# Kernel tuning notes

Hardware: AMD Instinct MI355X
Metric: run time of the kernel (lower is better)

## Reference

```python
import jax, jax.numpy as jnp
import numpy as np
from jax import lax

B, CI, CO, H, W = 8, 64, 64, 256, 256
M1 = M2 = 16
RANK, NEXP, SCALING = 4, 15, 0.1
G = 4  # expert_region_size = sqrt(num_experts + 1)
WF = W // 2 + 1

# expert i occupies grid cell (row, col) = ((i+1)//G, (i+1)%G); cell (0,0) is the base weights1 corner
_IDX = np.arange(1, NEXP + 1)
RR = jnp.asarray(_IDX // G)
CC = jnp.asarray(_IDX % G)


def setup_inputs() -> dict:
    key = jax.random.key(0)
    ks = jax.random.split(key, 20)
    rn = lambda k, shape, s: jax.random.normal(k, shape, jnp.float32) * s
    scale = 1.0 / (CI * CO)
    return {
        "x": rn(ks[0], (B, CI, H, W), 1.0),
        "w1_re": jax.random.uniform(ks[1], (CI, CO, M1, M2), jnp.float32) * scale,
        "w1_im": jax.random.uniform(ks[2], (CI, CO, M1, M2), jnp.float32) * scale,
        "w2_re": jax.random.uniform(ks[3], (CI, CO, M1, M2), jnp.float32) * scale,
        "w2_im": jax.random.uniform(ks[4], (CI, CO, M1, M2), jnp.float32) * scale,
        "la1_re": rn(ks[5], (NEXP, RANK, CI), 0.02),
        "la1_im": rn(ks[6], (NEXP, RANK, CI), 0.02),
        "lb1_re": rn(ks[7], (NEXP, CO, RANK, M1, M2), 0.02),
        "lb1_im": rn(ks[8], (NEXP, CO, RANK, M1, M2), 0.02),
        "la2_re": rn(ks[9], (NEXP, RANK, CI), 0.02),
        "la2_im": rn(ks[10], (NEXP, RANK, CI), 0.02),
        "lb2_re": rn(ks[11], (NEXP, CO, RANK, M1, M2), 0.02),
        "lb2_im": rn(ks[12], (NEXP, CO, RANK, M1, M2), 0.02),
        "gate1": rn(ks[13], (NEXP,), 0.1),
        "gate2": rn(ks[14], (NEXP,), 0.1),
    }


def reference(x, w1_re, w1_im, w2_re, w2_im,
              la1_re, la1_im, lb1_re, lb1_im,
              la2_re, la2_im, lb2_re, lb2_im,
              gate1, gate2):
    x_ft = jnp.fft.rfft2(x)  # [B, CI, H, WF] complex64

    # scalar gates (gate_on_data=False): sigmoid(gate / temperature), temperature=1
    g1 = jax.nn.sigmoid(gate1)  # [E]
    g2 = jax.nn.sigmoid(gate2)
    sploss = jnp.mean(g1) + jnp.mean(g2)

    w1 = lax.complex(w1_re, w1_im)
    w2 = lax.complex(w2_re, w2_im)
    la1 = lax.complex(la1_re, la1_im)
    lb1 = lax.complex(lb1_re, lb1_im)
    la2 = lax.complex(la2_re, la2_im)
    lb2 = lax.complex(lb2_re, lb2_im)

    # per-expert LoRA weights: sum_r lora_b[o,r,x,y] * lora_a[r,i] -> [E, I, O, M1, M2]
    lw1 = jnp.einsum("eri,eorxy->eioxy", la1, lb1) * SCALING
    lw2 = jnp.einsum("eri,eorxy->eioxy", la2, lb2) * SCALING

    # base corner products
    top_base = jnp.einsum("bixy,ioxy->boxy", x_ft[:, :, :M1, :M2], w1)
    bot_base = jnp.einsum("bixy,ioxy->boxy", x_ft[:, :, H - M1:, :M2], w2)

    # gather all expert input tiles at once via a GxG grid view of the low-freq corners
    top = x_ft[:, :, :G * M1, :G * M2].reshape(B, CI, G, M1, G, M2)
    topt = jnp.transpose(top, (2, 4, 0, 1, 3, 5))        # [G, G, B, CI, M1, M2]
    xe1 = topt[RR, CC]                                    # [E, B, CI, M1, M2]
    bot = x_ft[:, :, H - G * M1:, :G * M2].reshape(B, CI, G, M1, G, M2)
    bott = jnp.transpose(bot, (2, 4, 0, 1, 3, 5))
    xe2 = bott[G - 1 - RR, CC]  # rows H-row_end:H-row_start == bottom-grid block 3-row_idx

    oe1 = jnp.einsum("ebixy,eioxy->eboxy", xe1, lw1) * g1[:, None, None, None, None]
    oe2 = jnp.einsum("ebixy,eioxy->eboxy", xe2, lw2) * g2[:, None, None, None, None]

    # scatter all disjoint tiles back into out_ft
    out_top = jnp.zeros((G, G, B, CO, M1, M2), jnp.complex64)
    out_top = out_top.at[0, 0].set(top_base).at[RR, CC].set(oe1)
    out_bot = jnp.zeros((G, G, B, CO, M1, M2), jnp.complex64)
    out_bot = out_bot.at[G - 1, 0].set(bot_base).at[G - 1 - RR, CC].set(oe2)

    out_ft = jnp.zeros((B, CO, H, WF), jnp.complex64)
    top_full = jnp.transpose(out_top, (2, 3, 0, 4, 1, 5)).reshape(B, CO, G * M1, G * M2)
    bot_full = jnp.transpose(out_bot, (2, 3, 0, 4, 1, 5)).reshape(B, CO, G * M1, G * M2)
    out_ft = out_ft.at[:, :, :G * M1, :G * M2].set(top_full)
    out_ft = out_ft.at[:, :, H - G * M1:, :G * M2].set(bot_full)

    y = jnp.fft.irfft2(out_ft, s=(H, W))
    return (y, sploss)
```

## Files before the change

kernel.cpp:

```cpp
#include <hip/hip_runtime.h>
#include <math.h>

#define B_   8
#define CI_  64
#define CO_  64
#define H_   256
#define W_   256
#define NE_  15
#define RK_  4

typedef __attribute__((ext_vector_type(8))) short short8;
typedef __attribute__((ext_vector_type(4))) float f32x4;

__device__ __forceinline__ unsigned bf16u(float f) {
  return (__float_as_uint(f) + 0x8000u) >> 16;
}
__device__ __forceinline__ unsigned pk2(float lo, float hi) {
  return ((__float_as_uint(lo) + 0x8000u) >> 16) |
         ((__float_as_uint(hi) + 0x8000u) & 0xFFFF0000u);
}
__device__ __forceinline__ float ubf(unsigned short u) {
  return __uint_as_float(((unsigned)u) << 16);
}

__global__ __launch_bounds__(256) void kTab(unsigned short* __restrict__ TAt,
                                            unsigned short* __restrict__ TB,
                                            unsigned short* __restrict__ TD,
                                            unsigned short* __restrict__ TEt) {
  int idx = blockIdx.x * 256 + threadIdx.x;
  const float C = 6.28318530717958647692f / 256.f;
  if (idx < 32768) {
    int n = idx >> 8, q = idx & 255;
    int w = n >> 1, pl = n & 1;
    int mm = (q * w) & 255;
    float s, c; sincosf(C * (float)mm, &s, &c);
    TAt[idx] = (unsigned short)bf16u(pl ? -s : c);
    return;
  }
  idx -= 32768;
  if (idx < 131072) {
    int mrow = idx >> 9, k = idx & 511;
    int p = k >> 1, tt = k & 1;
    int hr = mrow & 127, imr = mrow >> 7;
    int h = (hr < 64) ? hr : hr + 128;
    int mm = (p * h) & 255;
    float s, c; sincosf(C * (float)mm, &s, &c);
    float v = (imr == 0) ? (tt == 0 ? c : s) : (tt == 0 ? -s : c);
    TB[idx] = (unsigned short)bf16u(v);
    return;
  }
  idx -= 131072;
  if (idx < 131072) {
    int mrow = idx >> 8, k = idx & 255;
    int hr = k >> 1, tt = k & 1;
    int p = mrow & 255, imr = mrow >> 8;
    int h = (hr < 64) ? hr : hr + 128;
    int mm = (p * h) & 255;
    float s, c; sincosf(C * (float)mm, &s, &c);
    float v = (imr == 0) ? (tt == 0 ? c : -s) : (tt == 0 ? s : c);
    TD[idx] = (unsigned short)bf16u(v);
    return;
  }
  idx -= 131072;
  if (idx < 32768) {
    int q = idx >> 7, k = idx & 127;
    int w = k >> 1, pl = k & 1;
    int mm = (q * w) & 255;
    float s, c; sincosf(C * (float)mm, &s, &c);
    float v = (pl == 0) ? ((w == 0 ? 1.f : 2.f * c) / 65536.f)
                        : ((w == 0 ? 0.f : -2.f * s) / 65536.f);
    TEt[idx] = (unsigned short)bf16u(v);
  }
}

__global__ __launch_bounds__(512, 4) void kAB(const float* __restrict__ x,
                                              const unsigned short* __restrict__ TAt,
                                              const unsigned short* __restrict__ TB,
                                              unsigned short* __restrict__ Xf) {
  __shared__ unsigned short As[256 * 32];
  __shared__ unsigned short Bs1[128 * 32];
  __shared__ unsigned short XcL[64 * 264];
  int t = threadIdx.x, lane = t & 63, wid = t >> 6;
  int bi = blockIdx.x;
  const float* xb = x + (size_t)bi * 65536;
  int lrow = lane & 15, lk = (lane >> 4) * 8;
  f32x4 acc2[2][4];
#pragma unroll
  for (int a = 0; a < 2; ++a)
#pragma unroll
    for (int b = 0; b < 4; ++b) acc2[a][b] = (f32x4){0.f, 0.f, 0.f, 0.f};

  for (int half = 0; half < 2; ++half) {
    f32x4 acc1[2][4];
#pragma unroll
    for (int a = 0; a < 2; ++a)
#pragma unroll
      for (int b = 0; b < 4; ++b) acc1[a][b] = (f32x4){0.f, 0.f, 0.f, 0.f};
    int mb1 = (wid >> 1) * 32, nb1 = (wid & 1) * 64;
    for (int kk = 0; kk < 8; ++kk) {
      int k0 = kk * 32;
      __syncthreads();
      {
        int r = t >> 2, hf = t & 3;
        const float* xp = xb + (size_t)(half * 128 + r) * 256 + k0 + hf * 8;
        float4 v0 = *(const float4*)(xp);
        float4 v1 = *(const float4*)(xp + 4);
        uint4 o;
        o.x = pk2(v0.x, v0.y); o.y = pk2(v0.z, v0.w);
        o.z = pk2(v1.x, v1.y); o.w = pk2(v1.z, v1.w);
        *(uint4*)&As[r * 32 + hf * 8] = o;
      }
      {
        int n = t >> 2, seg = t & 3;
        *(uint4*)&Bs1[n * 32 + seg * 8] = *(const uint4*)&TAt[n * 256 + k0 + seg * 8];
      }
      __syncthreads();
      short8 af[2], bf[4];
#pragma unroll
      for (int a = 0; a < 2; ++a)
        af[a] = *(const short8*)&As[(mb1 + a * 16 + lrow) * 32 + lk];
#pragma unroll
      for (int b = 0; b < 4; ++b)
        bf[b] = *(const short8*)&Bs1[(nb1 + b * 16 + lrow) * 32 + lk];
#pragma unroll
      for (int a = 0; a < 2; ++a)
#pragma unroll
        for (int b = 0; b < 4; ++b)
          acc1[a][b] = __builtin_amdgcn_mfma_f32_16x16x32_bf16(af[a], bf[b], acc1[a][b], 0, 0, 0);
    }
    __syncthreads();
#pragma unroll
    for (int a = 0; a < 2; ++a)
#pragma unroll
      for (int b = 0; b < 4; ++b)
#pragma unroll
        for (int r = 0; r < 4; ++r) {
          int m = mb1 + a * 16 + (lane >> 4) * 4 + r;
          int n = nb1 + b * 16 + lrow;
          XcL[(n >> 1) * 264 + 2 * m + (n & 1)] = (unsigned short)bf16u(acc1[a][b][r]);
        }
    __syncthreads();
    int mb2 = wid * 32;
    for (int kk = 0; kk < 8; ++kk) {
      int k0 = kk * 32;
      __syncthreads();
#pragma unroll
      for (int j = 0; j < 2; ++j) {
        int c = j * 512 + t;
        int m = c >> 2, seg = c & 3;
        *(uint4*)&As[m * 32 + seg * 8] =
            *(const uint4*)&TB[m * 512 + half * 256 + k0 + seg * 8];
      }
      __syncthreads();
      short8 af2[2], bf2[4];
#pragma unroll
      for (int a = 0; a < 2; ++a)
        af2[a] = *(const short8*)&As[(mb2 + a * 16 + lrow) * 32 + lk];
#pragma unroll
      for (int b = 0; b < 4; ++b)
        bf2[b] = *(const short8*)&XcL[(b * 16 + lrow) * 264 + k0 + lk];
#pragma unroll
      for (int a = 0; a < 2; ++a)
#pragma unroll
        for (int b = 0; b < 4; ++b)
          acc2[a][b] = __builtin_amdgcn_mfma_f32_16x16x32_bf16(af2[a], bf2[b], acc2[a][b], 0, 0, 0);
    }
  }
  unsigned short* dst = Xf + (size_t)bi * 16384;
#pragma unroll
  for (int a = 0; a < 2; ++a)
#pragma unroll
    for (int b = 0; b < 4; ++b)
#pragma unroll
      for (int r = 0; r < 4; ++r) {
        int m = wid * 32 + a * 16 + (lane >> 4) * 4 + r;
        int n = b * 16 + lrow;
        dst[m * 64 + n] = (unsigned short)bf16u(acc2[a][b][r]);
      }
}

__global__ __launch_bounds__(256) void kT(const unsigned short* __restrict__ Xf,
                                          float2* __restrict__ T,
                                          const float* __restrict__ la1re,
                                          const float* __restrict__ la1im,
                                          const float* __restrict__ la2re,
                                          const float* __restrict__ la2im) {
  int bid = blockIdx.x;
  int b = bid & 7;
  int e = (bid >> 3) % 15;
  int reg = bid / 120;
  int ep1 = e + 1;
  int grr = (reg == 0) ? (ep1 >> 2) : (3 - (ep1 >> 2));
  int gc = ep1 & 3;
  int hr0 = reg * 64 + grr * 16;
  int w0 = gc * 16;
  int t = threadIdx.x;
  int xx = t >> 4, yy = t & 15;
  const unsigned short* xp =
      Xf + (size_t)b * 64 * 16384 + (hr0 + xx) * 64 + (w0 + yy);
  const float* lare = (reg == 0) ? la1re : la2re;
  const float* laim = (reg == 0) ? la1im : la2im;
  float ar0 = 0.f, ai0 = 0.f, ar1 = 0.f, ai1 = 0.f;
  float ar2 = 0.f, ai2 = 0.f, ar3 = 0.f, ai3 = 0.f;
  for (int i = 0; i < 64; ++i) {
    float xr = ubf(xp[(size_t)i * 16384]);
    float xi = ubf(xp[(size_t)i * 16384 + 8192]);
    float l0r = lare[(e * 4 + 0) * 64 + i], l0i = laim[(e * 4 + 0) * 64 + i];
    float l1r = lare[(e * 4 + 1) * 64 + i], l1i = laim[(e * 4 + 1) * 64 + i];
    float l2r = lare[(e * 4 + 2) * 64 + i], l2i = laim[(e * 4 + 2) * 64 + i];
    float l3r = lare[(e * 4 + 3) * 64 + i], l3i = laim[(e * 4 + 3) * 64 + i];
    ar0 += l0r * xr - l0i * xi; ai0 += l0r * xi + l0i * xr;
    ar1 += l1r * xr - l1i * xi; ai1 += l1r * xi + l1i * xr;
    ar2 += l2r * xr - l2i * xi; ai2 += l2r * xi + l2i * xr;
    ar3 += l3r * xr - l3i * xi; ai3 += l3r * xi + l3i * xr;
  }
  float2* dst = T + ((((size_t)reg * 15 + e) * 8 + b) * 256 + t) * 4;
  dst[0] = make_float2(ar0, ai0);
  dst[1] = make_float2(ar1, ai1);
  dst[2] = make_float2(ar2, ai2);
  dst[3] = make_float2(ar3, ai3);
}

__global__ __launch_bounds__(256) void kDM(const unsigned short* __restrict__ Xf,
                                           const float2* __restrict__ T,
                                           unsigned short* __restrict__ Gt,
                                           const float* __restrict__ w1re,
                                           const float* __restrict__ w1im,
                                           const float* __restrict__ w2re,
                                           const float* __restrict__ w2im,
                                           const float* __restrict__ lb1re,
                                           const float* __restrict__ lb1im,
                                           const float* __restrict__ lb2re,
                                           const float* __restrict__ lb2im,
                                           const float* __restrict__ gate1,
                                           const float* __restrict__ gate2) {
  __shared__ unsigned Xs[32 * 4 * 8 * 8];
  if (blockIdx.x < 256) {
    int bid = blockIdx.x;
    int yc = bid & 1, xc = (bid >> 1) & 3, oc = (bid >> 3) & 15, reg = bid >> 7;
    int hrb = (reg == 0) ? xc * 4 : 112 + xc * 4;
    const float* Wre = (reg == 0) ? w1re : w2re;
    const float* Wim = (reg == 0) ? w1im : w2im;
    int t = threadIdx.x;
    int b = t >> 5, o = (t >> 3) & 3, yy = t & 7;
    int og = oc * 4 + o, yyg = yc * 8 + yy;
    float ar[4] = {0.f, 0.f, 0.f, 0.f}, ai[4] = {0.f, 0.f, 0.f, 0.f};
    for (int ch = 0; ch < 2; ++ch) {
      __syncthreads();
#pragma unroll
      for (int j = 0; j < 4; ++j) {
        int seg = t + j * 256;
        int sb = seg >> 7, sx = (seg >> 5) & 3, si = seg & 31;
        int i = ch * 32 + si;
        const unsigned short* p =
            Xf + (size_t)(sb * 64 + i) * 16384 + (hrb + sx) * 64 + yc * 8;
        uint4 re = *(const uint4*)p;
        uint4 im = *(const uint4*)(p + 8192);
        uint4 o0, o1;
        o0.x = (re.x & 0xFFFFu) | (im.x << 16);
        o0.y = (re.x >> 16) | (im.x & 0xFFFF0000u);
        o0.z = (re.y & 0xFFFFu) | (im.y << 16);
        o0.w = (re.y >> 16) | (im.y & 0xFFFF0000u);
        o1.x = (re.z & 0xFFFFu) | (im.z << 16);
        o1.y = (re.z >> 16) | (im.z & 0xFFFF0000u);
        o1.z = (re.w & 0xFFFFu) | (im.w << 16);
        o1.w = (re.w >> 16) | (im.w & 0xFFFF0000u);
        uint4* d = (uint4*)&Xs[((si * 4 + sx) * 8 + sb) * 8];
        d[0] = o0; d[1] = o1;
      }
      __syncthreads();
      for (int ic = 0; ic < 32; ++ic) {
        int i = ch * 32 + ic;
#pragma unroll
        for (int xs = 0; xs < 4; ++xs) {
          unsigned pk = Xs[((ic * 4 + xs) * 8 + b) * 8 + yy];
          float xr = ubf((unsigned short)(pk & 0xFFFFu));
          float xi = ubf((unsigned short)(pk >> 16));
          int widx = ((i * 64 + og) * 16 + xc * 4 + xs) * 16 + yyg;
          float wr = Wre[widx], wi = Wim[widx];
          ar[xs] += xr * wr - xi * wi;
          ai[xs] += xr * wi + xi * wr;
        }
      }
    }
    uint4 ov;
    ov.x = pk2(ar[0], ai[0]);
    ov.y = pk2(ar[1], ai[1]);
    ov.z = pk2(ar[2], ai[2]);
    ov.w = pk2(ar[3], ai[3]);
    *(uint4*)(Gt + ((size_t)(b * 64 + og) * 64 + yyg) * 256 + 2 * hrb) = ov;
  } else {
    int bid = blockIdx.x - 256;
    int xc = bid & 3, hrc = (bid >> 2) & 7, oc = bid >> 5;
    int t = threadIdx.x;
    int w = t & 63, og = t >> 6;
    int o = oc * 4 + og;
    int reg = hrc >> 2;
    int grr = hrc & 3;
    int gc = w >> 4, yy = w & 15;
    int e = (reg == 0) ? (4 * grr + gc - 1) : (4 * (3 - grr) + gc - 1);
    if (e < 0) return;
    float gate = (reg == 0) ? gate1[e] : gate2[e];
    float g = 0.1f / (1.f + __expf(-gate));
    const float* lbre = (reg == 0) ? lb1re : lb2re;
    const float* lbim = (reg == 0) ? lb1im : lb2im;
    size_t lbb = ((size_t)(e * 64 + o) * 4) * 256 + yy;
    float blr[4][4], bli[4][4];
#pragma unroll
    for (int x2 = 0; x2 < 4; ++x2) {
      int xx = xc * 4 + x2;
      const float* pr = lbre + lbb + xx * 16;
      const float* pi = lbim + lbb + xx * 16;
#pragma unroll
      for (int r = 0; r < 4; ++r) {
        blr[x2][r] = pr[r * 256];
        bli[x2][r] = pi[r * 256];
      }
    }
    const size_t tbase = (((size_t)reg * 15 + e) * 8) * 256 + yy;
    for (int b = 0; b < 8; ++b) {
      const float4* tp = (const float4*)(T + (tbase + (size_t)b * 256) * 4);
      unsigned out4[4];
#pragma unroll
      for (int x2 = 0; x2 < 4; ++x2) {
        int xx = xc * 4 + x2;
        float4 t01 = tp[xx * 32];
        float4 t23 = tp[xx * 32 + 1];
        float ar = 0.f, aim = 0.f;
        ar += t01.x * blr[x2][0] - t01.y * bli[x2][0];
        aim += t01.x * bli[x2][0] + t01.y * blr[x2][0];
        ar += t01.z * blr[x2][1] - t01.w * bli[x2][1];
        aim += t01.z * bli[x2][1] + t01.w * blr[x2][1];
        ar += t23.x * blr[x2][2] - t23.y * bli[x2][2];
        aim += t23.x * bli[x2][2] + t23.y * blr[x2][2];
        ar += t23.z * blr[x2][3] - t23.w * bli[x2][3];
        aim += t23.z * bli[x2][3] + t23.w * blr[x2][3];
        out4[x2] = pk2(g * ar, g * aim);
      }
      *(uint4*)(Gt + ((size_t)(b * 64 + o) * 64 + w) * 256 + hrc * 32 + xc * 8) =
          make_uint4(out4[0], out4[1], out4[2], out4[3]);
    }
  }
}

__global__ __launch_bounds__(512, 4) void kDE(const unsigned short* __restrict__ Gt,
                                              const unsigned short* __restrict__ TD,
                                              const unsigned short* __restrict__ TEt,
                                              float* __restrict__ y) {
  __shared__ __align__(16) char smem[77824];
  unsigned short* As  = (unsigned short*)smem;
  unsigned short* Bs  = (unsigned short*)(smem + 32768);
  unsigned short* ZL  = (unsigned short*)smem;
  unsigned short* Bs2 = (unsigned short*)(smem + 69632);
  int t = threadIdx.x, lane = t & 63, wid = t >> 6;
  int bo = blockIdx.x;
  const unsigned short* Grow = Gt + (size_t)bo * 16384;
  int lrow = lane & 15, lk = (lane >> 4) * 8;

  {
    int mb = wid * 64;
    f32x4 acc[4][4];
#pragma unroll
    for (int a = 0; a < 4; ++a)
#pragma unroll
      for (int b = 0; b < 4; ++b) acc[a][b] = (f32x4){0.f, 0.f, 0.f, 0.f};
    for (int kk = 0; kk < 8; ++kk) {
      int k0 = kk * 32;
      __syncthreads();
#pragma unroll
      for (int j = 0; j < 4; ++j) {
        int c = j * 512 + t;
        int m = c >> 2, seg = c & 3;
        *(uint4*)&As[m * 32 + seg * 8] = *(const uint4*)&TD[m * 256 + k0 + seg * 8];
      }
      if (t < 256) {
        int n = t >> 2, seg = t & 3;
        *(uint4*)&Bs[n * 32 + seg * 8] = *(const uint4*)&Grow[n * 256 + k0 + seg * 8];
      }
      __syncthreads();
      short8 af[4], bf[4];
#pragma unroll
      for (int a = 0; a < 4; ++a)
        af[a] = *(const short8*)&As[(mb + a * 16 + lrow) * 32 + lk];
#pragma unroll
      for (int b = 0; b < 4; ++b)
        bf[b] = *(const short8*)&Bs[(b * 16 + lrow) * 32 + lk];
#pragma unroll
      for (int a = 0; a < 4; ++a)
#pragma unroll
        for (int b = 0; b < 4; ++b)
          acc[a][b] = __builtin_amdgcn_mfma_f32_16x16x32_bf16(af[a], bf[b], acc[a][b], 0, 0, 0);
    }
    __syncthreads();
#pragma unroll
    for (int a = 0; a < 4; ++a)
#pragma unroll
      for (int b = 0; b < 4; ++b)
#pragma unroll
        for (int r = 0; r < 4; ++r) {
          int m = mb + a * 16 + (lane >> 4) * 4 + r;
          int p = m & 255, pl = m >> 8;
          int n = b * 16 + lrow;
          ZL[p * 136 + 2 * n + pl] = (unsigned short)bf16u(acc[a][b][r]);
        }
    __syncthreads();
  }

  int mb2 = (wid >> 1) * 64, nb2 = (wid & 1) * 64;
  for (int qh = 0; qh < 2; ++qh) {
    f32x4 acc[4][4];
#pragma unroll
    for (int a = 0; a < 4; ++a)
#pragma unroll
      for (int b = 0; b < 4; ++b) acc[a][b] = (f32x4){0.f, 0.f, 0.f, 0.f};
    for (int kk = 0; kk < 4; ++kk) {
      int k0 = kk * 32;
      __syncthreads();
      {
        int n = t >> 2, seg = t & 3;
        *(uint4*)&Bs2[n * 32 + seg * 8] =
            *(const uint4*)&TEt[(qh * 128 + n) * 128 + k0 + seg * 8];
      }
      __syncthreads();
      short8 af[4], bf[4];
#pragma unroll
      for (int a = 0; a < 4; ++a)
        af[a] = *(const short8*)&ZL[(mb2 + a * 16 + lrow) * 136 + k0 + lk];
#pragma unroll
      for (int b = 0; b < 4; ++b)
        bf[b] = *(const short8*)&Bs2[(nb2 + b * 16 + lrow) * 32 + lk];
#pragma unroll
      for (int a = 0; a < 4; ++a)
#pragma unroll
        for (int b = 0; b < 4; ++b)
          acc[a][b] = __builtin_amdgcn_mfma_f32_16x16x32_bf16(af[a], bf[b], acc[a][b], 0, 0, 0);
    }
    float* dst = y + (size_t)bo * 65536 + qh * 128;
#pragma unroll
    for (int a = 0; a < 4; ++a)
#pragma unroll
      for (int b = 0; b < 4; ++b)
#pragma unroll
        for (int r = 0; r < 4; ++r) {
          int p = mb2 + a * 16 + (lane >> 4) * 4 + r;
          int q = nb2 + b * 16 + lrow;
          dst[(size_t)p * 256 + q] = acc[a][b][r];
        }
  }
}

__global__ void kS2(const float* __restrict__ gate1, const float* __restrict__ gate2,
                    float* __restrict__ out) {
  if (threadIdx.x == 0) {
    float s = 0.f;
    for (int e = 0; e < NE_; ++e)
      s += 1.f / (1.f + expf(-gate1[e])) + 1.f / (1.f + expf(-gate2[e]));
    out[0] = s / (float)NE_;
  }
}

extern "C" void kernel_launch(void* const* d_in, const int* in_sizes, int n_in,
                              void* d_out, int out_size, void* d_ws, size_t ws_size,
                              hipStream_t stream) {
  const float* x     = (const float*)d_in[0];
  const float* w1re  = (const float*)d_in[1];
  const float* w1im  = (const float*)d_in[2];
  const float* w2re  = (const float*)d_in[3];
  const float* w2im  = (const float*)d_in[4];
  const float* la1re = (const float*)d_in[5];
  const float* la1im = (const float*)d_in[6];
  const float* lb1re = (const float*)d_in[7];
  const float* lb1im = (const float*)d_in[8];
  const float* la2re = (const float*)d_in[9];
  const float* la2im = (const float*)d_in[10];
  const float* lb2re = (const float*)d_in[11];
  const float* lb2im = (const float*)d_in[12];
  const float* gate1 = (const float*)d_in[13];
  const float* gate2 = (const float*)d_in[14];

  char* ws = (char*)d_ws;
  unsigned short* Xf  = (unsigned short*)(ws + ((size_t)32 << 20));
  unsigned short* Gt  = (unsigned short*)(ws + ((size_t)48 << 20));
  unsigned short* TAt = (unsigned short*)(ws + ((size_t)96 << 20));
  unsigned short* TB  = TAt + 32768;
  unsigned short* TD  = TB + 131072;
  unsigned short* TEt = TD + 131072;
  float2* Tw = (float2*)(ws + ((size_t)97 << 20));
  float* y = (float*)d_out;

  kTab<<<1280, 256, 0, stream>>>(TAt, TB, TD, TEt);
  kAB<<<512, 512, 0, stream>>>(x, TAt, TB, Xf);
  kT<<<240, 256, 0, stream>>>(Xf, Tw, la1re, la1im, la2re, la2im);
  kDM<<<768, 256, 0, stream>>>(Xf, Tw, Gt, w1re, w1im, w2re, w2im,
                               lb1re, lb1im, lb2re, lb2im, gate1, gate2);
  kDE<<<512, 512, 0, stream>>>(Gt, TD, TEt, y);
  kS2<<<1, 64, 0, stream>>>(gate1, gate2, y + (size_t)B_ * CO_ * H_ * W_);
}
```

Measured before the change: 395.9 us.

## Load MFMA operands directly from global memory, dropping LDS staging and barriers

In kAB and kDE the MFMA fragments are now read straight from global memory (twiddle tables, input x, Gt) rather than staged through shared-memory tiles guarded by __syncthreads in every k-step. kAB's first GEMM is regridded so each wave owns 16 rows across all 128 columns, converting x to bf16 in registers. The change removes LDS round trips and barriers but leans on L1/L2 caching for operand reuse across waves, with less coalesced 16-byte loads. It also drops the min-blocks launch bound and unrolls kC's reduction loop by 8.

New measurement: 471.9 us. +19.2%, slower.

```diff
diff --git a/kernel.cpp b/kernel.cpp
--- a/kernel.cpp
+++ b/kernel.cpp
@@ -73,12 +73,10 @@
   }
 }
 
-__global__ __launch_bounds__(512, 4) void kAB(const float* __restrict__ x,
-                                              const unsigned short* __restrict__ TAt,
-                                              const unsigned short* __restrict__ TB,
-                                              unsigned short* __restrict__ Xf) {
-  __shared__ unsigned short As[256 * 32];
-  __shared__ unsigned short Bs1[128 * 32];
+__global__ __launch_bounds__(512) void kAB(const float* __restrict__ x,
+                                           const unsigned short* __restrict__ TAt,
+                                           const unsigned short* __restrict__ TB,
+                                           unsigned short* __restrict__ Xf) {
   __shared__ unsigned short XcL[64 * 264];
   int t = threadIdx.x, lane = t & 63, wid = t >> 6;
   int bi = blockIdx.x;
@@ -91,71 +89,41 @@
     for (int b = 0; b < 4; ++b) acc2[a][b] = (f32x4){0.f, 0.f, 0.f, 0.f};
 
   for (int half = 0; half < 2; ++half) {
-    f32x4 acc1[2][4];
-#pragma unroll
-    for (int a = 0; a < 2; ++a)
-#pragma unroll
-      for (int b = 0; b < 4; ++b) acc1[a][b] = (f32x4){0.f, 0.f, 0.f, 0.f};
-    int mb1 = (wid >> 1) * 32, nb1 = (wid & 1) * 64;
+    f32x4 acc1[8];
+#pragma unroll
+    for (int b = 0; b < 8; ++b) acc1[b] = (f32x4){0.f, 0.f, 0.f, 0.f};
+    const float* xrow = xb + (size_t)(half * 128 + wid * 16 + lrow) * 256 + lk;
     for (int kk = 0; kk < 8; ++kk) {
       int k0 = kk * 32;
-      __syncthreads();
-      {
-        int r = t >> 2, hf = t & 3;
-        const float* xp = xb + (size_t)(half * 128 + r) * 256 + k0 + hf * 8;
-        float4 v0 = *(const float4*)(xp);
-        float4 v1 = *(const float4*)(xp + 4);
-        uint4 o;
-        o.x = pk2(v0.x, v0.y); o.y = pk2(v0.z, v0.w);
-        o.z = pk2(v1.x, v1.y); o.w = pk2(v1.z, v1.w);
-        *(uint4*)&As[r * 32 + hf * 8] = o;
-      }
-      {
-        int n = t >> 2, seg = t & 3;
-        *(uint4*)&Bs1[n * 32 + seg * 8] = *(const uint4*)&TAt[n * 256 + k0 + seg * 8];
-      }
-      __syncthreads();
-      short8 af[2], bf[4];
-#pragma unroll
-      for (int a = 0; a < 2; ++a)
-        af[a] = *(const short8*)&As[(mb1 + a * 16 + lrow) * 32 + lk];
-#pragma unroll
-      for (int b = 0; b < 4; ++b)
-        bf[b] = *(const short8*)&Bs1[(nb1 + b * 16 + lrow) * 32 + lk];
-#pragma unroll
-      for (int a = 0; a < 2; ++a)
-#pragma unroll
-        for (int b = 0; b < 4; ++b)
-          acc1[a][b] = __builtin_amdgcn_mfma_f32_16x16x32_bf16(af[a], bf[b], acc1[a][b], 0, 0, 0);
+      float4 v0 = *(const float4*)(xrow + k0);
+      float4 v1 = *(const float4*)(xrow + k0 + 4);
+      union { short8 s; unsigned u[4]; } afu;
+      afu.u[0] = pk2(v0.x, v0.y); afu.u[1] = pk2(v0.z, v0.w);
+      afu.u[2] = pk2(v1.x, v1.y); afu.u[3] = pk2(v1.z, v1.w);
+      short8 af = afu.s;
+#pragma unroll
+      for (int b = 0; b < 8; ++b) {
+        short8 bf = *(const short8*)&TAt[(b * 16 + lrow) * 256 + k0 + lk];
+        acc1[b] = __builtin_amdgcn_mfma_f32_16x16x32_bf16(af, bf, acc1[b], 0, 0, 0);
+      }
     }
     __syncthreads();
 #pragma unroll
-    for (int a = 0; a < 2; ++a)
-#pragma unroll
-      for (int b = 0; b < 4; ++b)
-#pragma unroll
-        for (int r = 0; r < 4; ++r) {
-          int m = mb1 + a * 16 + (lane >> 4) * 4 + r;
-          int n = nb1 + b * 16 + lrow;
-          XcL[(n >> 1) * 264 + 2 * m + (n & 1)] = (unsigned short)bf16u(acc1[a][b][r]);
-        }
+    for (int b = 0; b < 8; ++b)
+#pragma unroll
+      for (int r = 0; r < 4; ++r) {
+        int m = wid * 16 + (lane >> 4) * 4 + r;
+        int n = b * 16 + lrow;
+        XcL[(n >> 1) * 264 + 2 * m + (n & 1)] = (unsigned short)bf16u(acc1[b][r]);
+      }
     __syncthreads();
     int mb2 = wid * 32;
     for (int kk = 0; kk < 8; ++kk) {
       int k0 = kk * 32;
-      __syncthreads();
-#pragma unroll
-      for (int j = 0; j < 2; ++j) {
-        int c = j * 512 + t;
-        int m = c >> 2, seg = c & 3;
-        *(uint4*)&As[m * 32 + seg * 8] =
-            *(const uint4*)&TB[m * 512 + half * 256 + k0 + seg * 8];
-      }
-      __syncthreads();
       short8 af2[2], bf2[4];
 #pragma unroll
       for (int a = 0; a < 2; ++a)
-        af2[a] = *(const short8*)&As[(mb2 + a * 16 + lrow) * 32 + lk];
+        af2[a] = *(const short8*)&TB[(mb2 + a * 16 + lrow) * 512 + half * 256 + k0 + lk];
 #pragma unroll
       for (int b = 0; b < 4; ++b)
         bf2[b] = *(const short8*)&XcL[(b * 16 + lrow) * 264 + k0 + lk];
@@ -202,6 +170,7 @@
   const float* laim = (reg == 0) ? la1im : la2im;
   float ar0 = 0.f, ai0 = 0.f, ar1 = 0.f, ai1 = 0.f;
   float ar2 = 0.f, ai2 = 0.f, ar3 = 0.f, ai3 = 0.f;
+#pragma unroll 8
   for (int i = 0; i < 64; ++i) {
     float xr = ubf(xp[(size_t)i * 16384]);
     float xi = ubf(xp[(size_t)i * 16384 + 8192]);
@@ -343,15 +312,11 @@
   }
 }
 
-__global__ __launch_bounds__(512, 4) void kDE(const unsigned short* __restrict__ Gt,
-                                              const unsigned short* __restrict__ TD,
-                                              const unsigned short* __restrict__ TEt,
-                                              float* __restrict__ y) {
-  __shared__ __align__(16) char smem[77824];
-  unsigned short* As  = (unsigned short*)smem;
-  unsigned short* Bs  = (unsigned short*)(smem + 32768);
-  unsigned short* ZL  = (unsigned short*)smem;
-  unsigned short* Bs2 = (unsigned short*)(smem + 69632);
+__global__ __launch_bounds__(512) void kDE(const unsigned short* __restrict__ Gt,
+                                           const unsigned short* __restrict__ TD,
+                                           const unsigned short* __restrict__ TEt,
+                                           float* __restrict__ y) {
+  __shared__ unsigned short ZL[256 * 136];
   int t = threadIdx.x, lane = t & 63, wid = t >> 6;
   int bo = blockIdx.x;
   const unsigned short* Grow = Gt + (size_t)bo * 16384;
@@ -366,32 +331,19 @@
       for (int b = 0; b < 4; ++b) acc[a][b] = (f32x4){0.f, 0.f, 0.f, 0.f};
     for (int kk = 0; kk < 8; ++kk) {
       int k0 = kk * 32;
-      __syncthreads();
-#pragma unroll
-      for (int j = 0; j < 4; ++j) {
-        int c = j * 512 + t;
-        int m = c >> 2, seg = c & 3;
-        *(uint4*)&As[m * 32 + seg * 8] = *(const uint4*)&TD[m * 256 + k0 + seg * 8];
-      }
-      if (t < 256) {
-        int n = t >> 2, seg = t & 3;
-        *(uint4*)&Bs[n * 32 + seg * 8] = *(const uint4*)&Grow[n * 256 + k0 + seg * 8];
-      }
-      __syncthreads();
       short8 af[4], bf[4];
 #pragma unroll
       for (int a = 0; a < 4; ++a)
-        af[a] = *(const short8*)&As[(mb + a * 16 + lrow) * 32 + lk];
+        af[a] = *(const short8*)&TD[(mb + a * 16 + lrow) * 256 + k0 + lk];
 #pragma unroll
       for (int b = 0; b < 4; ++b)
-        bf[b] = *(const short8*)&Bs[(b * 16 + lrow) * 32 + lk];
+        bf[b] = *(const short8*)&Grow[(b * 16 + lrow) * 256 + k0 + lk];
 #pragma unroll
       for (int a = 0; a < 4; ++a)
 #pragma unroll
         for (int b = 0; b < 4; ++b)
           acc[a][b] = __builtin_amdgcn_mfma_f32_16x16x32_bf16(af[a], bf[b], acc[a][b], 0, 0, 0);
     }
-    __syncthreads();
 #pragma unroll
     for (int a = 0; a < 4; ++a)
 #pragma unroll
@@ -415,20 +367,13 @@
       for (int b = 0; b < 4; ++b) acc[a][b] = (f32x4){0.f, 0.f, 0.f, 0.f};
     for (int kk = 0; kk < 4; ++kk) {
       int k0 = kk * 32;
-      __syncthreads();
-      {
-        int n = t >> 2, seg = t & 3;
-        *(uint4*)&Bs2[n * 32 + seg * 8] =
-            *(const uint4*)&TEt[(qh * 128 + n) * 128 + k0 + seg * 8];
-      }
-      __syncthreads();
       short8 af[4], bf[4];
 #pragma unroll
       for (int a = 0; a < 4; ++a)
         af[a] = *(const short8*)&ZL[(mb2 + a * 16 + lrow) * 136 + k0 + lk];
 #pragma unroll
       for (int b = 0; b < 4; ++b)
-        bf[b] = *(const short8*)&Bs2[(nb2 + b * 16 + lrow) * 32 + lk];
+        bf[b] = *(const short8*)&TEt[(qh * 128 + nb2 + b * 16 + lrow) * 128 + k0 + lk];
 #pragma unroll
       for (int a = 0; a < 4; ++a)
 #pragma unroll
```

## Use direct global-to-LDS loads with XOR-swizzled tiles and K=64 steps in DFT GEMMs

Applied to the files above, without the earlier changes.

Table and spectrum tiles in kAB and kDE are now loaded with the global_load_lds builtin, so they go straight to shared memory instead of through registers. Tiles are stored with an XOR swizzle to avoid LDS bank conflicts. kAB now takes K in steps of 64, which halves the number of barrier pairs, and the minimum-occupancy launch bound is dropped. Together these aim to cut LDS conflicts, VGPR staging and synchronisation overhead, at the cost of more complex addressing and possibly lower occupancy.

After: 387.2 us. -2.2%, faster.

```diff
diff --git a/kernel.cpp b/kernel.cpp
--- a/kernel.cpp
+++ b/kernel.cpp
@@ -21,6 +21,11 @@
 }
 __device__ __forceinline__ float ubf(unsigned short u) {
   return __uint_as_float(((unsigned)u) << 16);
+}
+__device__ __forceinline__ void gload16(const void* g, void* l) {
+  __builtin_amdgcn_global_load_lds(
+      (const __attribute__((address_space(1))) unsigned int*)g,
+      (__attribute__((address_space(3))) unsigned int*)l, 16, 0, 0);
 }
 
 __global__ __launch_bounds__(256) void kTab(unsigned short* __restrict__ TAt,
@@ -73,17 +78,16 @@
   }
 }
 
-__global__ __launch_bounds__(512, 4) void kAB(const float* __restrict__ x,
-                                              const unsigned short* __restrict__ TAt,
-                                              const unsigned short* __restrict__ TB,
-                                              unsigned short* __restrict__ Xf) {
-  __shared__ unsigned short As[256 * 32];
-  __shared__ unsigned short Bs1[128 * 32];
+__global__ __launch_bounds__(512) void kAB(const float* __restrict__ x,
+                                           const unsigned short* __restrict__ TAt,
+                                           const unsigned short* __restrict__ TB,
+                                           unsigned short* __restrict__ Xf) {
+  __shared__ unsigned short As[16384];
   __shared__ unsigned short XcL[64 * 264];
   int t = threadIdx.x, lane = t & 63, wid = t >> 6;
   int bi = blockIdx.x;
   const float* xb = x + (size_t)bi * 65536;
-  int lrow = lane & 15, lk = (lane >> 4) * 8;
+  int lrow = lane & 15, lk = (lane >> 4) * 8, jhi = lane >> 4;
   f32x4 acc2[2][4];
 #pragma unroll
   for (int a = 0; a < 2; ++a)
@@ -97,36 +101,46 @@
 #pragma unroll
       for (int b = 0; b < 4; ++b) acc1[a][b] = (f32x4){0.f, 0.f, 0.f, 0.f};
     int mb1 = (wid >> 1) * 32, nb1 = (wid & 1) * 64;
-    for (int kk = 0; kk < 8; ++kk) {
-      int k0 = kk * 32;
-      __syncthreads();
-      {
-        int r = t >> 2, hf = t & 3;
-        const float* xp = xb + (size_t)(half * 128 + r) * 256 + k0 + hf * 8;
-        float4 v0 = *(const float4*)(xp);
-        float4 v1 = *(const float4*)(xp + 4);
-        uint4 o;
-        o.x = pk2(v0.x, v0.y); o.y = pk2(v0.z, v0.w);
-        o.z = pk2(v1.x, v1.y); o.w = pk2(v1.z, v1.w);
-        *(uint4*)&As[r * 32 + hf * 8] = o;
-      }
-      {
-        int n = t >> 2, seg = t & 3;
-        *(uint4*)&Bs1[n * 32 + seg * 8] = *(const uint4*)&TAt[n * 256 + k0 + seg * 8];
-      }
-      __syncthreads();
-      short8 af[2], bf[4];
-#pragma unroll
-      for (int a = 0; a < 2; ++a)
-        af[a] = *(const short8*)&As[(mb1 + a * 16 + lrow) * 32 + lk];
-#pragma unroll
-      for (int b = 0; b < 4; ++b)
-        bf[b] = *(const short8*)&Bs1[(nb1 + b * 16 + lrow) * 32 + lk];
-#pragma unroll
-      for (int a = 0; a < 2; ++a)
-#pragma unroll
-        for (int b = 0; b < 4; ++b)
-          acc1[a][b] = __builtin_amdgcn_mfma_f32_16x16x32_bf16(af[a], bf[b], acc1[a][b], 0, 0, 0);
+    for (int kk = 0; kk < 4; ++kk) {
+      int k0 = kk * 64;
+      __syncthreads();
+#pragma unroll
+      for (int j = 0; j < 2; ++j) {
+        int c = j * 512 + t;
+        int r = c >> 3, seg = c & 7;
+        int ssw = (seg ^ (r & 7)) * 8;
+        {
+          const float* xp = xb + (size_t)(half * 128 + r) * 256 + k0 + ssw;
+          float4 v0 = *(const float4*)(xp);
+          float4 v1 = *(const float4*)(xp + 4);
+          uint4 o;
+          o.x = pk2(v0.x, v0.y); o.y = pk2(v0.z, v0.w);
+          o.z = pk2(v1.x, v1.y); o.w = pk2(v1.z, v1.w);
+          *(uint4*)&As[r * 64 + seg * 8] = o;
+        }
+        gload16(&TAt[r * 256 + k0 + ssw], &As[8192 + c * 8]);
+      }
+      __syncthreads();
+#pragma unroll
+      for (int k2 = 0; k2 < 64; k2 += 32) {
+        int jb = (k2 >> 3) + jhi;
+        short8 af[2], bf[4];
+#pragma unroll
+        for (int a = 0; a < 2; ++a) {
+          int row = mb1 + a * 16 + lrow;
+          af[a] = *(const short8*)&As[row * 64 + ((jb ^ (row & 7))) * 8];
+        }
+#pragma unroll
+        for (int b = 0; b < 4; ++b) {
+          int row = nb1 + b * 16 + lrow;
+          bf[b] = *(const short8*)&As[8192 + row * 64 + ((jb ^ (row & 7))) * 8];
+        }
+#pragma unroll
+        for (int a = 0; a < 2; ++a)
+#pragma unroll
+          for (int b = 0; b < 4; ++b)
+            acc1[a][b] = __builtin_amdgcn_mfma_f32_16x16x32_bf16(af[a], bf[b], acc1[a][b], 0, 0, 0);
+      }
     }
     __syncthreads();
 #pragma unroll
@@ -141,29 +155,35 @@
         }
     __syncthreads();
     int mb2 = wid * 32;
-    for (int kk = 0; kk < 8; ++kk) {
-      int k0 = kk * 32;
-      __syncthreads();
-#pragma unroll
-      for (int j = 0; j < 2; ++j) {
+    for (int kk = 0; kk < 4; ++kk) {
+      int k0 = kk * 64;
+      __syncthreads();
+#pragma unroll
+      for (int j = 0; j < 4; ++j) {
         int c = j * 512 + t;
-        int m = c >> 2, seg = c & 3;
-        *(uint4*)&As[m * 32 + seg * 8] =
-            *(const uint4*)&TB[m * 512 + half * 256 + k0 + seg * 8];
-      }
-      __syncthreads();
-      short8 af2[2], bf2[4];
-#pragma unroll
-      for (int a = 0; a < 2; ++a)
-        af2[a] = *(const short8*)&As[(mb2 + a * 16 + lrow) * 32 + lk];
-#pragma unroll
-      for (int b = 0; b < 4; ++b)
-        bf2[b] = *(const short8*)&XcL[(b * 16 + lrow) * 264 + k0 + lk];
-#pragma unroll
-      for (int a = 0; a < 2; ++a)
+        int m = c >> 3, seg = c & 7;
+        int ssw = (seg ^ (m & 7)) * 8;
+        gload16(&TB[m * 512 + half * 256 + k0 + ssw], &As[c * 8]);
+      }
+      __syncthreads();
+#pragma unroll
+      for (int k2 = 0; k2 < 64; k2 += 32) {
+        int jb = (k2 >> 3) + jhi;
+        short8 af2[2], bf2[4];
+#pragma unroll
+        for (int a = 0; a < 2; ++a) {
+          int row = mb2 + a * 16 + lrow;
+          af2[a] = *(const short8*)&As[row * 64 + ((jb ^ (row & 7))) * 8];
+        }
 #pragma unroll
         for (int b = 0; b < 4; ++b)
-          acc2[a][b] = __builtin_amdgcn_mfma_f32_16x16x32_bf16(af2[a], bf2[b], acc2[a][b], 0, 0, 0);
+          bf2[b] = *(const short8*)&XcL[(b * 16 + lrow) * 264 + k0 + k2 + lk];
+#pragma unroll
+        for (int a = 0; a < 2; ++a)
+#pragma unroll
+          for (int b = 0; b < 4; ++b)
+            acc2[a][b] = __builtin_amdgcn_mfma_f32_16x16x32_bf16(af2[a], bf2[b], acc2[a][b], 0, 0, 0);
+      }
     }
   }
   unsigned short* dst = Xf + (size_t)bi * 16384;
@@ -202,6 +222,7 @@
   const float* laim = (reg == 0) ? la1im : la2im;
   float ar0 = 0.f, ai0 = 0.f, ar1 = 0.f, ai1 = 0.f;
   float ar2 = 0.f, ai2 = 0.f, ar3 = 0.f, ai3 = 0.f;
+#pragma unroll 8
   for (int i = 0; i < 64; ++i) {
     float xr = ubf(xp[(size_t)i * 16384]);
     float xi = ubf(xp[(size_t)i * 16384 + 8192]);
@@ -343,10 +364,10 @@
   }
 }
 
-__global__ __launch_bounds__(512, 4) void kDE(const unsigned short* __restrict__ Gt,
-                                              const unsigned short* __restrict__ TD,
-                                              const unsigned short* __restrict__ TEt,
-                                              float* __restrict__ y) {
+__global__ __launch_bounds__(512) void kDE(const unsigned short* __restrict__ Gt,
+                                           const unsigned short* __restrict__ TD,
+                                           const unsigned short* __restrict__ TEt,
+                                           float* __restrict__ y) {
   __shared__ __align__(16) char smem[77824];
   unsigned short* As  = (unsigned short*)smem;
   unsigned short* Bs  = (unsigned short*)(smem + 32768);
@@ -355,7 +376,7 @@
   int t = threadIdx.x, lane = t & 63, wid = t >> 6;
   int bo = blockIdx.x;
   const unsigned short* Grow = Gt + (size_t)bo * 16384;
-  int lrow = lane & 15, lk = (lane >> 4) * 8;
+  int lrow = lane & 15, lk = (lane >> 4) * 8, jhi = lane >> 4;
 
   {
     int mb = wid * 64;
@@ -371,20 +392,24 @@
       for (int j = 0; j < 4; ++j) {
         int c = j * 512 + t;
         int m = c >> 2, seg = c & 3;
-        *(uint4*)&As[m * 32 + seg * 8] = *(const uint4*)&TD[m * 256 + k0 + seg * 8];
+        gload16(&TD[m * 256 + k0 + ((seg ^ (m & 3))) * 8], &As[c * 8]);
       }
       if (t < 256) {
         int n = t >> 2, seg = t & 3;
-        *(uint4*)&Bs[n * 32 + seg * 8] = *(const uint4*)&Grow[n * 256 + k0 + seg * 8];
+        gload16(&Grow[n * 256 + k0 + ((seg ^ (n & 3))) * 8], &Bs[t * 8]);
       }
       __syncthreads();
       short8 af[4], bf[4];
 #pragma unroll
-      for (int a = 0; a < 4; ++a)
-        af[a] = *(const short8*)&As[(mb + a * 16 + lrow) * 32 + lk];
-#pragma unroll
-      for (int b = 0; b < 4; ++b)
-        bf[b] = *(const short8*)&Bs[(b * 16 + lrow) * 32 + lk];
+      for (int a = 0; a < 4; ++a) {
+        int row = mb + a * 16 + lrow;
+        af[a] = *(const short8*)&As[row * 32 + ((jhi ^ (row & 3))) * 8];
+      }
+#pragma unroll
+      for (int b = 0; b < 4; ++b) {
+        int row = b * 16 + lrow;
+        bf[b] = *(const short8*)&Bs[row * 32 + ((jhi ^ (row & 3))) * 8];
+      }
 #pragma unroll
       for (int a = 0; a < 4; ++a)
 #pragma unroll
@@ -418,8 +443,7 @@
       __syncthreads();
       {
         int n = t >> 2, seg = t & 3;
-        *(uint4*)&Bs2[n * 32 + seg * 8] =
-            *(const uint4*)&TEt[(qh * 128 + n) * 128 + k0 + seg * 8];
+        gload16(&TEt[(qh * 128 + n) * 128 + k0 + ((seg ^ (n & 3))) * 8], &Bs2[t * 8]);
       }
       __syncthreads();
       short8 af[4], bf[4];
@@ -427,8 +451,10 @@
       for (int a = 0; a < 4; ++a)
         af[a] = *(const short8*)&ZL[(mb2 + a * 16 + lrow) * 136 + k0 + lk];
 #pragma unroll
-      for (int b = 0; b < 4; ++b)
-        bf[b] = *(const short8*)&Bs2[(nb2 + b * 16 + lrow) * 32 + lk];
+      for (int b = 0; b < 4; ++b) {
+        int row = nb2 + b * 16 + lrow;
+        bf[b] = *(const short8*)&Bs2[row * 32 + ((jhi ^ (row & 3))) * 8];
+      }
 #pragma unroll
       for (int a = 0; a < 4; ++a)
 #pragma unroll
```
